# Performance work log

Hardware: AMD Instinct MI355X
Metric: run time of the kernel (lower is better)

The kernel has to match this reference:

```python
import jax, jax.numpy as jnp
import numpy as np

DIM = 192
NUM_HEADS = 6
WINDOW = (2, 6, 12)
INPUT_RES = (8, 48, 180)
TYPE_OF_WINDOWS = (INPUT_RES[0] // WINDOW[0]) * (INPUT_RES[1] // WINDOW[1])  # 32
N_TOK = WINDOW[0] * WINDOW[1] * WINDOW[2]  # 144
NLON = INPUT_RES[2] // WINDOW[2]  # 15
TABLE_ROWS = WINDOW[0] ** 2 * WINDOW[1] ** 2 * (2 * WINDOW[2] - 1)  # 3312


def calculate_position_bias_indices(ws):
    wz, wh, ww = ws
    zi = np.arange(wz)
    zj = -np.arange(wz) * wz
    hi = np.arange(wh)
    hj = -np.arange(wh) * wh
    w = np.arange(ww)
    c1 = np.stack(np.meshgrid(zi, hi, w, indexing='ij')).reshape(3, -1)
    c2 = np.stack(np.meshgrid(zj, hj, w, indexing='ij')).reshape(3, -1)
    coords = (c1[:, :, None] - c2[:, None, :]).transpose(1, 2, 0).copy()
    coords[:, :, 2] += ww - 1
    coords[:, :, 1] *= 2 * ww - 1
    coords[:, :, 0] *= (2 * ww - 1) * wh * wh
    return coords.sum(-1)  # (N, N) in [0, TABLE_ROWS)


def setup_inputs() -> dict:
    key = jax.random.key(0)
    ks = jax.random.split(key, 7)
    B_ = NLON  # batch=1 times nLon window columns
    x = jax.random.normal(ks[0], (B_, TYPE_OF_WINDOWS, N_TOK, DIM), dtype=jnp.float32)
    mask = jax.random.normal(ks[1], (NLON, TYPE_OF_WINDOWS, N_TOK, N_TOK), dtype=jnp.float32)
    qkv_w = jax.random.normal(ks[2], (3 * DIM, DIM), dtype=jnp.float32) * 0.02
    qkv_b = jax.random.normal(ks[3], (3 * DIM,), dtype=jnp.float32) * 0.02
    proj_w = jax.random.normal(ks[4], (DIM, DIM), dtype=jnp.float32) * 0.02
    proj_b = jax.random.normal(ks[5], (DIM,), dtype=jnp.float32) * 0.02
    bias_table = jax.random.normal(ks[6], (TABLE_ROWS, TYPE_OF_WINDOWS, NUM_HEADS), dtype=jnp.float32) * 0.02
    position_index = jnp.asarray(calculate_position_bias_indices(WINDOW), dtype=jnp.int64)
    return {"x": x, "mask": mask, "qkv_w": qkv_w, "qkv_b": qkv_b,
            "proj_w": proj_w, "proj_b": proj_b, "bias_table": bias_table,
            "position_index": position_index}


def reference(x, mask, qkv_w, qkv_b, proj_w, proj_b, bias_table, position_index):
    B_, nW_, N, C = x.shape
    H = NUM_HEADS
    hd = C // H
    scale = hd ** (-0.5)
    # qkv projection: (B_, nW_, N, 3, H, hd)
    qkv = (jnp.einsum('bwnc,dc->bwnd', x, qkv_w) + qkv_b).reshape(B_, nW_, N, 3, H, hd)
    q = qkv[:, :, :, 0] * scale  # (B_, nW_, N, H, hd)
    k = qkv[:, :, :, 1]
    v = qkv[:, :, :, 2]
    # attention scores: (B_, H, nW_, N, N)
    attn = jnp.einsum('bwihd,bwjhd->bhwij', q, k)
    # gathered earth position bias -> (H, nW_, N, N)
    bias = bias_table[position_index.reshape(-1)]  # (N*N, nW_, H)
    bias = bias.reshape(N, N, nW_, H).transpose(3, 2, 0, 1)
    attn = attn + bias[None]
    # mask add: view (B_//nLon, nLon, H, nW_, N, N) + mask (nLon, 1, nW_, N, N)
    nLon = mask.shape[0]
    attn = attn.reshape(B_ // nLon, nLon, H, nW_, N, N) + mask[None, :, None]
    attn = attn.reshape(B_, H, nW_, N, N)
    attn = jax.nn.softmax(attn, axis=-1)
    out = jnp.einsum('bhwij,bwjhd->bwihd', attn, v).reshape(B_, nW_, N, C)
    out = jnp.einsum('bwnc,dc->bwnd', out, proj_w) + proj_b
    return out
```

## Files before the change

kernel.cpp:

```cpp
#include <hip/hip_runtime.h>
#include <hip/hip_bf16.h>

#define B_LON 15
#define NW    32
#define NTOK  144
#define DIM   192
#define NH    6
#define HD    32
#define K3    576
#define MROWS (B_LON*NW*NTOK)
#define NN    (NTOK*NTOK)
#define SCALE 0.17677669529663687f

typedef __attribute__((ext_vector_type(8))) short bf16x8;
typedef __attribute__((ext_vector_type(8))) unsigned short u16x8;
typedef __attribute__((ext_vector_type(4))) float f32x4;

__device__ inline unsigned short f2bf(float f) {
  __bf16 h = (__bf16)f;
  return __builtin_bit_cast(unsigned short, h);
}
__device__ inline float bf2f(unsigned short u) {
  union { unsigned int i; float f; } c;
  c.i = ((unsigned int)u) << 16;
  return c.f;
}

#define NX8 1658880
#define NQ8 13824
#define NP8 4608

__global__ __launch_bounds__(256) void conv_bf_k(
    const float* __restrict__ x, const float* __restrict__ qw,
    const float* __restrict__ pw,
    unsigned short* __restrict__ xbf, unsigned short* __restrict__ qwbf,
    unsigned short* __restrict__ pwbf) {
  const long gid = (long)blockIdx.x * 256 + threadIdx.x;
  const float* src;
  unsigned short* dst;
  long off;
  if (gid < NX8)            { src = x;  dst = xbf;  off = gid; }
  else if (gid < NX8 + NQ8) { src = qw; dst = qwbf; off = gid - NX8; }
  else                      { src = pw; dst = pwbf; off = gid - NX8 - NQ8; }
  const float4 a = ((const float4*)src)[off * 2];
  const float4 b = ((const float4*)src)[off * 2 + 1];
  u16x8 u = {f2bf(a.x), f2bf(a.y), f2bf(a.z), f2bf(a.w),
             f2bf(b.x), f2bf(b.y), f2bf(b.z), f2bf(b.w)};
  *(u16x8*)&dst[off * 8] = u;
}

__global__ __launch_bounds__(256) void bias_pre_k(
    const float* __restrict__ btab, const int* __restrict__ pos,
    unsigned short* __restrict__ biasb) {
  const int wh  = blockIdx.x;
  const int seg = blockIdx.y * 2304;
  unsigned short* dst = biasb + (size_t)wh * NN;
#pragma unroll
  for (int it = 0; it < 9; ++it) {
    const int e = seg + it * 256 + threadIdx.x;
    dst[e] = f2bf(btab[(size_t)pos[e] * (NW * NH) + wh]);
  }
}

__global__ __launch_bounds__(256) void qkv_gemm_k(
    const unsigned short* __restrict__ X, const unsigned short* __restrict__ W,
    const float* __restrict__ Bv,
    unsigned short* __restrict__ qb, unsigned short* __restrict__ kb,
    unsigned short* __restrict__ vb) {
  __shared__ unsigned short As[256 * 72];
  __shared__ unsigned short Bs[64 * 72];
  const int t    = threadIdx.x;
  const int n0   = blockIdx.x * 64;
  const int m0   = blockIdx.y * 256;
  const int w    = t >> 6;
  const int lane = t & 63;
  const int ln15 = lane & 15;
  const int quad = lane >> 4;
  const int srow = t >> 3;
  const int schk = (t & 7) * 8;

  f32x4 acc[4][4];
#pragma unroll
  for (int i = 0; i < 4; ++i)
#pragma unroll
    for (int j = 0; j < 4; ++j) acc[i][j] = (f32x4){0.f, 0.f, 0.f, 0.f};

  for (int k0 = 0; k0 < 192; k0 += 64) {
    u16x8 ar[8], br[2];
#pragma unroll
    for (int rr = 0; rr < 8; ++rr)
      ar[rr] = *(const u16x8*)&X[(size_t)(m0 + rr * 32 + srow) * 192 + k0 + schk];
#pragma unroll
    for (int rr = 0; rr < 2; ++rr)
      br[rr] = *(const u16x8*)&W[(size_t)(n0 + rr * 32 + srow) * 192 + k0 + schk];
    __syncthreads();
#pragma unroll
    for (int rr = 0; rr < 8; ++rr)
      *(u16x8*)&As[(rr * 32 + srow) * 72 + schk] = ar[rr];
#pragma unroll
    for (int rr = 0; rr < 2; ++rr)
      *(u16x8*)&Bs[(rr * 32 + srow) * 72 + schk] = br[rr];
    __syncthreads();

#pragma unroll
    for (int half = 0; half < 2; ++half) {
      bf16x8 af[4], bf[4];
#pragma unroll
      for (int mt = 0; mt < 4; ++mt)
        af[mt] = *(bf16x8*)&As[(w * 64 + mt * 16 + ln15) * 72 + half * 32 + quad * 8];
#pragma unroll
      for (int nt = 0; nt < 4; ++nt)
        bf[nt] = *(bf16x8*)&Bs[(nt * 16 + ln15) * 72 + half * 32 + quad * 8];
#pragma unroll
      for (int mt = 0; mt < 4; ++mt)
#pragma unroll
        for (int nt = 0; nt < 4; ++nt)
          acc[mt][nt] = __builtin_amdgcn_mfma_f32_16x16x32_bf16(
              af[mt], bf[nt], acc[mt][nt], 0, 0, 0);
    }
    __syncthreads();
  }

  const int s   = n0 / 192;
  const int nr  = n0 % 192;
  const float sc2 = (s == 0) ? SCALE : 1.0f;
  unsigned short* dst = (s == 0) ? qb : (s == 1 ? kb : vb);
#pragma unroll
  for (int nt = 0; nt < 4; ++nt) {
    const int colg = n0 + nt * 16 + ln15;
    const int h    = (nr + nt * 16 + ln15) >> 5;
    const int dd   = (nr + nt * 16 + ln15) & 31;
    const float bias = Bv[colg];
#pragma unroll
    for (int mt = 0; mt < 4; ++mt) {
#pragma unroll
      for (int r = 0; r < 4; ++r) {
        const int m  = m0 + w * 64 + mt * 16 + quad * 4 + r;
        const int bw = m / NTOK;
        const int n  = m % NTOK;
        const unsigned short val = f2bf((acc[mt][nt][r] + bias) * sc2);
        if (s < 2)
          dst[((size_t)(bw * NH + h) * NTOK + n) * HD + dd] = val;
        else
          dst[((size_t)(bw * NH + h) * HD + dd) * NTOK + n] = val;
      }
    }
  }
}

__global__ __launch_bounds__(192, 3) void attn_k(
    const unsigned short* __restrict__ qbuf, const unsigned short* __restrict__ kbuf,
    const unsigned short* __restrict__ vbuf, const float* __restrict__ mask,
    const unsigned short* __restrict__ biasb, unsigned short* __restrict__ ao) {
  __shared__ unsigned short Ks[NTOK * 36];
  __shared__ unsigned short Vs[32 * 160];
  __shared__ unsigned short Ps[3 * 16 * 168];

  const int t    = threadIdx.x;
  const int wave = t / 64;
  const int lane = t & 63;
  const int ln15 = lane & 15;
  const int quad = lane >> 4;
  const int idx  = blockIdx.x;
  const int h    = idx / 480;
  const int bw   = idx % 480;
  const int w    = bw & 31;
  const int wh   = w * NH + h;
  const size_t hb = (size_t)(bw * NH + h) * (NTOK * HD);
  const unsigned short* qh = qbuf + hb;
  const float* maskp = mask + (size_t)bw * NN;
  const unsigned short* biasp = biasb + (size_t)wh * NN;
  unsigned short* ps = &Ps[wave * 16 * 168];

  for (int it = t; it < 576; it += 192) {
    const int row = it >> 2;
    const int col = (it & 3) * 8;
    *(u16x8*)&Ks[row * 36 + col] = *(const u16x8*)&kbuf[hb + row * HD + col];
  }
  for (int it = t; it < 576; it += 192) {
    const int row = it / 18;
    const int col = (it % 18) * 8;
    *(u16x8*)&Vs[row * 160 + col] = *(const u16x8*)&vbuf[hb + row * NTOK + col];
  }
  if (t < 64) {
    u16x8 z = {0, 0, 0, 0, 0, 0, 0, 0};
    *(u16x8*)&Vs[(t >> 1) * 160 + 144 + (t & 1) * 8] = z;
  }
  {
    ushort4 z = {0, 0, 0, 0};
    *(ushort4*)&ps[(lane >> 2) * 168 + 144 + (lane & 3) * 4] = z;
  }
  __syncthreads();

  for (int g = wave * 3; g < wave * 3 + 3; ++g) {
    const int i0 = g * 16;
    const int ib = i0 + quad * 4;

    const bf16x8 qf = *(const bf16x8*)&qh[(i0 + ln15) * HD + quad * 8];
    f32x4 s[9];
#pragma unroll
    for (int jt = 0; jt < 9; ++jt) {
      const bf16x8 kf = *(const bf16x8*)&Ks[(jt * 16 + ln15) * 36 + quad * 8];
      s[jt] = (f32x4){0.f, 0.f, 0.f, 0.f};
      s[jt] = __builtin_amdgcn_mfma_f32_16x16x32_bf16(qf, kf, s[jt], 0, 0, 0);
    }

#pragma unroll
    for (int jt = 0; jt < 9; ++jt) {
      const int j = jt * 16 + ln15;
#pragma unroll
      for (int r = 0; r < 4; ++r) {
        const int ij = (ib + r) * NTOK + j;
        s[jt][r] += bf2f(biasp[ij]) + maskp[ij];
      }
    }

    float rinv[4];
#pragma unroll
    for (int r = 0; r < 4; ++r) {
      float mx = s[0][r];
#pragma unroll
      for (int jt = 1; jt < 9; ++jt) mx = fmaxf(mx, s[jt][r]);
#pragma unroll
      for (int off = 1; off < 16; off <<= 1) mx = fmaxf(mx, __shfl_xor(mx, off));
      float sum = 0.f;
#pragma unroll
      for (int jt = 0; jt < 9; ++jt) {
        const float e = __expf(s[jt][r] - mx);
        s[jt][r] = e;
        sum += e;
      }
#pragma unroll
      for (int off = 1; off < 16; off <<= 1) sum += __shfl_xor(sum, off);
      rinv[r] = 1.0f / sum;
    }

#pragma unroll
    for (int jt = 0; jt < 9; ++jt)
#pragma unroll
      for (int r = 0; r < 4; ++r)
        ps[(quad * 4 + r) * 168 + jt * 16 + ln15] = f2bf(s[jt][r]);

    f32x4 o[2] = {{0.f, 0.f, 0.f, 0.f}, {0.f, 0.f, 0.f, 0.f}};
#pragma unroll
    for (int kt = 0; kt < 5; ++kt) {
      const bf16x8 pf = *(const bf16x8*)&ps[ln15 * 168 + kt * 32 + quad * 8];
#pragma unroll
      for (int nt = 0; nt < 2; ++nt) {
        const bf16x8 vf = *(const bf16x8*)&Vs[(nt * 16 + ln15) * 160 + kt * 32 + quad * 8];
        o[nt] = __builtin_amdgcn_mfma_f32_16x16x32_bf16(pf, vf, o[nt], 0, 0, 0);
      }
    }

#pragma unroll
    for (int nt = 0; nt < 2; ++nt)
#pragma unroll
      for (int r = 0; r < 4; ++r)
        ao[(size_t)(bw * NTOK + ib + r) * DIM + h * HD + nt * 16 + ln15] =
            f2bf(o[nt][r] * rinv[r]);
  }
}

__global__ __launch_bounds__(256) void proj_gemm_k(
    const unsigned short* __restrict__ AO, const unsigned short* __restrict__ W,
    const float* __restrict__ Bv, float* __restrict__ out) {
  __shared__ unsigned short As[256 * 72];
  __shared__ unsigned short Bs[64 * 72];
  const int t    = threadIdx.x;
  const int n0   = blockIdx.x * 64;
  const int m0   = blockIdx.y * 256;
  const int w    = t >> 6;
  const int lane = t & 63;
  const int ln15 = lane & 15;
  const int quad = lane >> 4;
  const int srow = t >> 3;
  const int schk = (t & 7) * 8;

  f32x4 acc[4][4];
#pragma unroll
  for (int i = 0; i < 4; ++i)
#pragma unroll
    for (int j = 0; j < 4; ++j) acc[i][j] = (f32x4){0.f, 0.f, 0.f, 0.f};

  for (int k0 = 0; k0 < 192; k0 += 64) {
    u16x8 ar[8], br[2];
#pragma unroll
    for (int rr = 0; rr < 8; ++rr)
      ar[rr] = *(const u16x8*)&AO[(size_t)(m0 + rr * 32 + srow) * 192 + k0 + schk];
#pragma unroll
    for (int rr = 0; rr < 2; ++rr)
      br[rr] = *(const u16x8*)&W[(size_t)(n0 + rr * 32 + srow) * 192 + k0 + schk];
    __syncthreads();
#pragma unroll
    for (int rr = 0; rr < 8; ++rr)
      *(u16x8*)&As[(rr * 32 + srow) * 72 + schk] = ar[rr];
#pragma unroll
    for (int rr = 0; rr < 2; ++rr)
      *(u16x8*)&Bs[(rr * 32 + srow) * 72 + schk] = br[rr];
    __syncthreads();

#pragma unroll
    for (int half = 0; half < 2; ++half) {
      bf16x8 af[4], bf[4];
#pragma unroll
      for (int mt = 0; mt < 4; ++mt)
        af[mt] = *(bf16x8*)&As[(w * 64 + mt * 16 + ln15) * 72 + half * 32 + quad * 8];
#pragma unroll
      for (int nt = 0; nt < 4; ++nt)
        bf[nt] = *(bf16x8*)&Bs[(nt * 16 + ln15) * 72 + half * 32 + quad * 8];
#pragma unroll
      for (int mt = 0; mt < 4; ++mt)
#pragma unroll
        for (int nt = 0; nt < 4; ++nt)
          acc[mt][nt] = __builtin_amdgcn_mfma_f32_16x16x32_bf16(
              af[mt], bf[nt], acc[mt][nt], 0, 0, 0);
    }
    __syncthreads();
  }

#pragma unroll
  for (int nt = 0; nt < 4; ++nt) {
    const int colg = n0 + nt * 16 + ln15;
    const float bias = Bv[colg];
#pragma unroll
    for (int mt = 0; mt < 4; ++mt) {
#pragma unroll
      for (int r = 0; r < 4; ++r) {
        const int m = m0 + w * 64 + mt * 16 + quad * 4 + r;
        out[(size_t)m * 192 + colg] = acc[mt][nt][r] + bias;
      }
    }
  }
}

extern "C" void kernel_launch(void* const* d_in, const int* in_sizes, int n_in,
                              void* d_out, int out_size, void* d_ws, size_t ws_size,
                              hipStream_t stream) {
  const float* x      = (const float*)d_in[0];
  const float* mask   = (const float*)d_in[1];
  const float* qkv_w  = (const float*)d_in[2];
  const float* qkv_b  = (const float*)d_in[3];
  const float* proj_w = (const float*)d_in[4];
  const float* proj_b = (const float*)d_in[5];
  const float* btab   = (const float*)d_in[6];
  const int*   pos    = (const int*)d_in[7];
  float* out = (float*)d_out;

  unsigned short* ws = (unsigned short*)d_ws;
  const size_t sz = (size_t)MROWS * DIM;
  unsigned short* qbuf  = ws;
  unsigned short* kbuf  = ws + sz;
  unsigned short* vbuf  = ws + 2 * sz;
  unsigned short* aobuf = ws + 3 * sz + 256;
  unsigned short* biasb = ws + 4 * sz + 1024;
  unsigned short* xbf   = biasb + (size_t)192 * NN;
  unsigned short* qwbf  = xbf + sz;
  unsigned short* pwbf  = qwbf + (size_t)K3 * DIM;

  conv_bf_k<<<NX8 / 256 + NQ8 / 256 + NP8 / 256, 256, 0, stream>>>(
      x, qkv_w, proj_w, xbf, qwbf, pwbf);
  bias_pre_k<<<dim3(NW * NH, 9), 256, 0, stream>>>(btab, pos, biasb);
  qkv_gemm_k<<<dim3(K3 / 64, MROWS / 256), 256, 0, stream>>>(
      xbf, qwbf, qkv_b, qbuf, kbuf, vbuf);
  attn_k<<<NH * 480, 192, 0, stream>>>(
      qbuf, kbuf, vbuf, mask, biasb, aobuf);
  proj_gemm_k<<<dim3(DIM / 64, MROWS / 256), 256, 0, stream>>>(
      aobuf, pwbf, proj_b, out);
}
```

Before: 304.5 us.

## Fuse x fp32-to-bf16 conversion into QKV GEMM and restructure GEMM tiling

The separate conversion pass over x is dropped. The QKV GEMM now reads fp32 x directly and converts it to bf16 while staging a full 128x192 row tile in LDS. Both the QKV and projection GEMMs change to one block per 128-row M tile that loops over all N columns, reading weights straight from global memory/L2 instead of staging them in LDS. This removes a full write and read of the bf16 copy of x and re-reads A only once per block, at the cost of fewer blocks, uncached weight fragment loads, and a serial N loop per block.

```diff
diff --git a/kernel.cpp b/kernel.cpp
--- a/kernel.cpp
+++ b/kernel.cpp
@@ -26,22 +26,18 @@
   return c.f;
 }
 
-#define NX8 1658880
 #define NQ8 13824
 #define NP8 4608
 
 __global__ __launch_bounds__(256) void conv_bf_k(
-    const float* __restrict__ x, const float* __restrict__ qw,
-    const float* __restrict__ pw,
-    unsigned short* __restrict__ xbf, unsigned short* __restrict__ qwbf,
-    unsigned short* __restrict__ pwbf) {
+    const float* __restrict__ qw, const float* __restrict__ pw,
+    unsigned short* __restrict__ qwbf, unsigned short* __restrict__ pwbf) {
   const long gid = (long)blockIdx.x * 256 + threadIdx.x;
   const float* src;
   unsigned short* dst;
   long off;
-  if (gid < NX8)            { src = x;  dst = xbf;  off = gid; }
-  else if (gid < NX8 + NQ8) { src = qw; dst = qwbf; off = gid - NX8; }
-  else                      { src = pw; dst = pwbf; off = gid - NX8 - NQ8; }
+  if (gid < NQ8) { src = qw; dst = qwbf; off = gid; }
+  else           { src = pw; dst = pwbf; off = gid - NQ8; }
   const float4 a = ((const float4*)src)[off * 2];
   const float4 b = ((const float4*)src)[off * 2 + 1];
   u16x8 u = {f2bf(a.x), f2bf(a.y), f2bf(a.z), f2bf(a.w),
@@ -63,86 +59,82 @@
 }
 
 __global__ __launch_bounds__(256) void qkv_gemm_k(
-    const unsigned short* __restrict__ X, const unsigned short* __restrict__ W,
+    const float* __restrict__ X, const unsigned short* __restrict__ W,
     const float* __restrict__ Bv,
     unsigned short* __restrict__ qb, unsigned short* __restrict__ kb,
     unsigned short* __restrict__ vb) {
-  __shared__ unsigned short As[256 * 72];
-  __shared__ unsigned short Bs[64 * 72];
+  __shared__ unsigned short As[128 * 200];
   const int t    = threadIdx.x;
-  const int n0   = blockIdx.x * 64;
-  const int m0   = blockIdx.y * 256;
+  const int m0   = blockIdx.x * 128;
   const int w    = t >> 6;
   const int lane = t & 63;
   const int ln15 = lane & 15;
   const int quad = lane >> 4;
-  const int srow = t >> 3;
-  const int schk = (t & 7) * 8;
-
-  f32x4 acc[4][4];
-#pragma unroll
-  for (int i = 0; i < 4; ++i)
-#pragma unroll
-    for (int j = 0; j < 4; ++j) acc[i][j] = (f32x4){0.f, 0.f, 0.f, 0.f};
-
-  for (int k0 = 0; k0 < 192; k0 += 64) {
-    u16x8 ar[8], br[2];
-#pragma unroll
-    for (int rr = 0; rr < 8; ++rr)
-      ar[rr] = *(const u16x8*)&X[(size_t)(m0 + rr * 32 + srow) * 192 + k0 + schk];
-#pragma unroll
-    for (int rr = 0; rr < 2; ++rr)
-      br[rr] = *(const u16x8*)&W[(size_t)(n0 + rr * 32 + srow) * 192 + k0 + schk];
-    __syncthreads();
-#pragma unroll
-    for (int rr = 0; rr < 8; ++rr)
-      *(u16x8*)&As[(rr * 32 + srow) * 72 + schk] = ar[rr];
-#pragma unroll
-    for (int rr = 0; rr < 2; ++rr)
-      *(u16x8*)&Bs[(rr * 32 + srow) * 72 + schk] = br[rr];
-    __syncthreads();
-
-#pragma unroll
-    for (int half = 0; half < 2; ++half) {
-      bf16x8 af[4], bf[4];
+  const int wm   = (w & 1) * 64;
+  const int wn   = (w >> 1) * 32;
+
+  for (int it = t; it < 3072; it += 256) {
+    const int row = it / 24;
+    const int c8  = (it % 24) * 8;
+    const float4 a = *(const float4*)(X + (size_t)(m0 + row) * 192 + c8);
+    const float4 b = *(const float4*)(X + (size_t)(m0 + row) * 192 + c8 + 4);
+    u16x8 u = {f2bf(a.x), f2bf(a.y), f2bf(a.z), f2bf(a.w),
+               f2bf(b.x), f2bf(b.y), f2bf(b.z), f2bf(b.w)};
+    *(u16x8*)&As[row * 200 + c8] = u;
+  }
+  __syncthreads();
+
+  for (int nt = 0; nt < 9; ++nt) {
+    const int col16_0 = nt * 64 + wn;
+
+    f32x4 acc[4][2];
+#pragma unroll
+    for (int mt = 0; mt < 4; ++mt)
+#pragma unroll
+      for (int ntj = 0; ntj < 2; ++ntj) acc[mt][ntj] = (f32x4){0.f, 0.f, 0.f, 0.f};
+
+#pragma unroll
+    for (int ks = 0; ks < 6; ++ks) {
+      bf16x8 bf[2];
+#pragma unroll
+      for (int ntj = 0; ntj < 2; ++ntj)
+        bf[ntj] = *(const bf16x8*)&W[(size_t)(col16_0 + ntj * 16 + ln15) * 192 +
+                                     ks * 32 + quad * 8];
+      bf16x8 af[4];
 #pragma unroll
       for (int mt = 0; mt < 4; ++mt)
-        af[mt] = *(bf16x8*)&As[(w * 64 + mt * 16 + ln15) * 72 + half * 32 + quad * 8];
-#pragma unroll
-      for (int nt = 0; nt < 4; ++nt)
-        bf[nt] = *(bf16x8*)&Bs[(nt * 16 + ln15) * 72 + half * 32 + quad * 8];
+        af[mt] = *(bf16x8*)&As[(wm + mt * 16 + ln15) * 200 + ks * 32 + quad * 8];
 #pragma unroll
       for (int mt = 0; mt < 4; ++mt)
 #pragma unroll
-        for (int nt = 0; nt < 4; ++nt)
-          acc[mt][nt] = __builtin_amdgcn_mfma_f32_16x16x32_bf16(
-              af[mt], bf[nt], acc[mt][nt], 0, 0, 0);
-    }
-    __syncthreads();
-  }
-
-  const int s   = n0 / 192;
-  const int nr  = n0 % 192;
-  const float sc2 = (s == 0) ? SCALE : 1.0f;
-  unsigned short* dst = (s == 0) ? qb : (s == 1 ? kb : vb);
-#pragma unroll
-  for (int nt = 0; nt < 4; ++nt) {
-    const int colg = n0 + nt * 16 + ln15;
-    const int h    = (nr + nt * 16 + ln15) >> 5;
-    const int dd   = (nr + nt * 16 + ln15) & 31;
-    const float bias = Bv[colg];
-#pragma unroll
-    for (int mt = 0; mt < 4; ++mt) {
-#pragma unroll
-      for (int r = 0; r < 4; ++r) {
-        const int m  = m0 + w * 64 + mt * 16 + quad * 4 + r;
-        const int bw = m / NTOK;
-        const int n  = m % NTOK;
-        const unsigned short val = f2bf((acc[mt][nt][r] + bias) * sc2);
-        if (s < 2)
-          dst[((size_t)(bw * NH + h) * NTOK + n) * HD + dd] = val;
-        else
-          dst[((size_t)(bw * NH + h) * HD + dd) * NTOK + n] = val;
+        for (int ntj = 0; ntj < 2; ++ntj)
+          acc[mt][ntj] = __builtin_amdgcn_mfma_f32_16x16x32_bf16(
+              af[mt], bf[ntj], acc[mt][ntj], 0, 0, 0);
+    }
+
+#pragma unroll
+    for (int ntj = 0; ntj < 2; ++ntj) {
+      const int col16 = col16_0 + ntj * 16;
+      const int s     = col16 / 192;
+      const int rem16 = col16 % 192;
+      const int h     = (rem16 + ln15) >> 5;
+      const int dd    = (rem16 + ln15) & 31;
+      const float sc2 = (s == 0) ? SCALE : 1.0f;
+      const float bias = Bv[col16 + ln15];
+      unsigned short* dst = (s == 0) ? qb : (s == 1 ? kb : vb);
+#pragma unroll
+      for (int mt = 0; mt < 4; ++mt) {
+#pragma unroll
+        for (int r = 0; r < 4; ++r) {
+          const int m  = m0 + wm + mt * 16 + quad * 4 + r;
+          const int bw = m / NTOK;
+          const int n  = m % NTOK;
+          const unsigned short val = f2bf((acc[mt][ntj][r] + bias) * sc2);
+          if (s < 2)
+            dst[((size_t)(bw * NH + h) * NTOK + n) * HD + dd] = val;
+          else
+            dst[((size_t)(bw * NH + h) * HD + dd) * NTOK + n] = val;
+        }
       }
     }
   }
@@ -264,70 +256,63 @@
 __global__ __launch_bounds__(256) void proj_gemm_k(
     const unsigned short* __restrict__ AO, const unsigned short* __restrict__ W,
     const float* __restrict__ Bv, float* __restrict__ out) {
-  __shared__ unsigned short As[256 * 72];
-  __shared__ unsigned short Bs[64 * 72];
+  __shared__ unsigned short As[128 * 200];
   const int t    = threadIdx.x;
-  const int n0   = blockIdx.x * 64;
-  const int m0   = blockIdx.y * 256;
+  const int m0   = blockIdx.x * 128;
   const int w    = t >> 6;
   const int lane = t & 63;
   const int ln15 = lane & 15;
   const int quad = lane >> 4;
-  const int srow = t >> 3;
-  const int schk = (t & 7) * 8;
-
-  f32x4 acc[4][4];
-#pragma unroll
-  for (int i = 0; i < 4; ++i)
-#pragma unroll
-    for (int j = 0; j < 4; ++j) acc[i][j] = (f32x4){0.f, 0.f, 0.f, 0.f};
-
-  for (int k0 = 0; k0 < 192; k0 += 64) {
-    u16x8 ar[8], br[2];
-#pragma unroll
-    for (int rr = 0; rr < 8; ++rr)
-      ar[rr] = *(const u16x8*)&AO[(size_t)(m0 + rr * 32 + srow) * 192 + k0 + schk];
-#pragma unroll
-    for (int rr = 0; rr < 2; ++rr)
-      br[rr] = *(const u16x8*)&W[(size_t)(n0 + rr * 32 + srow) * 192 + k0 + schk];
-    __syncthreads();
-#pragma unroll
-    for (int rr = 0; rr < 8; ++rr)
-      *(u16x8*)&As[(rr * 32 + srow) * 72 + schk] = ar[rr];
-#pragma unroll
-    for (int rr = 0; rr < 2; ++rr)
-      *(u16x8*)&Bs[(rr * 32 + srow) * 72 + schk] = br[rr];
-    __syncthreads();
-
-#pragma unroll
-    for (int half = 0; half < 2; ++half) {
-      bf16x8 af[4], bf[4];
+  const int wm   = (w & 1) * 64;
+  const int wn   = (w >> 1) * 32;
+
+  for (int it = t; it < 3072; it += 256) {
+    const int row = it / 24;
+    const int c8  = (it % 24) * 8;
+    *(u16x8*)&As[row * 200 + c8] =
+        *(const u16x8*)&AO[(size_t)(m0 + row) * 192 + c8];
+  }
+  __syncthreads();
+
+  for (int nt = 0; nt < 3; ++nt) {
+    const int col16_0 = nt * 64 + wn;
+
+    f32x4 acc[4][2];
+#pragma unroll
+    for (int mt = 0; mt < 4; ++mt)
+#pragma unroll
+      for (int ntj = 0; ntj < 2; ++ntj) acc[mt][ntj] = (f32x4){0.f, 0.f, 0.f, 0.f};
+
+#pragma unroll
+    for (int ks = 0; ks < 6; ++ks) {
+      bf16x8 bf[2];
+#pragma unroll
+      for (int ntj = 0; ntj < 2; ++ntj)
+        bf[ntj] = *(const bf16x8*)&W[(size_t)(col16_0 + ntj * 16 + ln15) * 192 +
+                                     ks * 32 + quad * 8];
+      bf16x8 af[4];
 #pragma unroll
       for (int mt = 0; mt < 4; ++mt)
-        af[mt] = *(bf16x8*)&As[(w * 64 + mt * 16 + ln15) * 72 + half * 32 + quad * 8];
-#pragma unroll
-      for (int nt = 0; nt < 4; ++nt)
-        bf[nt] = *(bf16x8*)&Bs[(nt * 16 + ln15) * 72 + half * 32 + quad * 8];
+        af[mt] = *(bf16x8*)&As[(wm + mt * 16 + ln15) * 200 + ks * 32 + quad * 8];
 #pragma unroll
       for (int mt = 0; mt < 4; ++mt)
 #pragma unroll
-        for (int nt = 0; nt < 4; ++nt)
-          acc[mt][nt] = __builtin_amdgcn_mfma_f32_16x16x32_bf16(
-              af[mt], bf[nt], acc[mt][nt], 0, 0, 0);
-    }
-    __syncthreads();
-  }
-
-#pragma unroll
-  for (int nt = 0; nt < 4; ++nt) {
-    const int colg = n0 + nt * 16 + ln15;
-    const float bias = Bv[colg];
-#pragma unroll
-    for (int mt = 0; mt < 4; ++mt) {
-#pragma unroll
-      for (int r = 0; r < 4; ++r) {
-        const int m = m0 + w * 64 + mt * 16 + quad * 4 + r;
-        out[(size_t)m * 192 + colg] = acc[mt][nt][r] + bias;
+        for (int ntj = 0; ntj < 2; ++ntj)
+          acc[mt][ntj] = __builtin_amdgcn_mfma_f32_16x16x32_bf16(
+              af[mt], bf[ntj], acc[mt][ntj], 0, 0, 0);
+    }
+
+#pragma unroll
+    for (int ntj = 0; ntj < 2; ++ntj) {
+      const int colg = col16_0 + ntj * 16 + ln15;
+      const float bias = Bv[colg];
+#pragma unroll
+      for (int mt = 0; mt < 4; ++mt) {
+#pragma unroll
+        for (int r = 0; r < 4; ++r) {
+          const int m = m0 + wm + mt * 16 + quad * 4 + r;
+          out[(size_t)m * 192 + colg] = acc[mt][ntj][r] + bias;
+        }
       }
     }
   }
@@ -353,17 +338,15 @@
   unsigned short* vbuf  = ws + 2 * sz;
   unsigned short* aobuf = ws + 3 * sz + 256;
   unsigned short* biasb = ws + 4 * sz + 1024;
-  unsigned short* xbf   = biasb + (size_t)192 * NN;
-  unsigned short* qwbf  = xbf + sz;
+  unsigned short* qwbf  = biasb + (size_t)192 * NN;
   unsigned short* pwbf  = qwbf + (size_t)K3 * DIM;
 
-  conv_bf_k<<<NX8 / 256 + NQ8 / 256 + NP8 / 256, 256, 0, stream>>>(
-      x, qkv_w, proj_w, xbf, qwbf, pwbf);
+  conv_bf_k<<<(NQ8 + NP8) / 256, 256, 0, stream>>>(qkv_w, proj_w, qwbf, pwbf);
   bias_pre_k<<<dim3(NW * NH, 9), 256, 0, stream>>>(btab, pos, biasb);
-  qkv_gemm_k<<<dim3(K3 / 64, MROWS / 256), 256, 0, stream>>>(
-      xbf, qwbf, qkv_b, qbuf, kbuf, vbuf);
+  qkv_gemm_k<<<MROWS / 128, 256, 0, stream>>>(
+      x, qwbf, qkv_b, qbuf, kbuf, vbuf);
   attn_k<<<NH * 480, 192, 0, stream>>>(
       qbuf, kbuf, vbuf, mask, biasb, aobuf);
-  proj_gemm_k<<<dim3(DIM / 64, MROWS / 256), 256, 0, stream>>>(
+  proj_gemm_k<<<MROWS / 128, 256, 0, stream>>>(
       aobuf, pwbf, proj_b, out);
 }
```

Measured after the change: 347.8 us. 14.2% more time.
